# Kernel tuning notes

Hardware: AMD Instinct MI355X
Metric: run time of the kernel (lower is better)

## Reference

```python
import jax, jax.numpy as jnp
import numpy as np

CODEBOOK_SIZE = 8192
TOKEN_SIZE = 256
COMMITMENT_COST = 0.25
B, C, H, W = 32, 256, 32, 32


def setup_inputs() -> dict:
    key = jax.random.key(0)
    k1, k2 = jax.random.split(key)
    z = jax.random.normal(k1, (B, C, H, W), dtype=jnp.float32)
    # torch init: uniform_(-1/codebook_size, 1/codebook_size)
    embedding = jax.random.uniform(
        k2, (CODEBOOK_SIZE, TOKEN_SIZE), dtype=jnp.float32,
        minval=-1.0 / CODEBOOK_SIZE, maxval=1.0 / CODEBOOK_SIZE)
    return {"z": z, "embedding": embedding}


def reference(z, embedding):
    # b c h w -> b h w c
    z = jnp.transpose(z.astype(jnp.float32), (0, 2, 3, 1))
    b, h, w, c = z.shape
    z_flat = z.reshape(-1, c)  # [N, c]

    # squared euclidean distances: ||z||^2 + ||e||^2 - 2 z e^T
    d = (jnp.sum(z_flat ** 2, axis=1, keepdims=True)
         + jnp.sum(embedding ** 2, axis=1)
         - 2.0 * jnp.einsum('nd,kd->nk', z_flat, embedding))  # [N, K]
    idx = jnp.argmin(d, axis=1)  # [N]

    z_q = embedding[idx].reshape(z.shape)  # [b,h,w,c]

    commitment_loss = COMMITMENT_COST * jnp.mean(
        (jax.lax.stop_gradient(z_q) - z) ** 2)
    codebook_loss = jnp.mean((z_q - jax.lax.stop_gradient(z)) ** 2)
    loss = commitment_loss + codebook_loss

    # straight-through estimator
    z_q_st = z + jax.lax.stop_gradient(z_q - z)
    z_q_out = jnp.transpose(z_q_st, (0, 3, 1, 2))  # b h w c -> b c h w

    min_encoding_indices = idx.reshape(b, h, w)
    return (z_q_out, loss, commitment_loss, codebook_loss,
            min_encoding_indices)
```

## Files before the change

### kernel.cpp

```cpp
#include <hip/hip_runtime.h>
#include <float.h>

#define NBATCH 32
#define NCHAN  256
#define NHW    1024
#define NTOK   32768
#define NK     8192
#define ND     256
#define ZELEMS 8388608
#define OUT_LOSS 8388608
#define OUT_IDX  8388611
#define MARGIN   1.2e-4f

typedef short bf16x8  __attribute__((ext_vector_type(8)));
typedef float f32x4   __attribute__((ext_vector_type(4)));
typedef float f32x16  __attribute__((ext_vector_type(16)));

__device__ __forceinline__ unsigned short f2bf(float f) {
    unsigned int u = __float_as_uint(f);
    u += 0x7FFFu + ((u >> 16) & 1u);
    return (unsigned short)(u >> 16);
}

__device__ __forceinline__ float embed8(float x, int code) {
    return __int_as_float((__float_as_int(x) & 0xFFFFFF00) | code);
}


__global__ __launch_bounds__(256) void k_cast(const float* __restrict__ zg,
                                              const float* __restrict__ E,
                                              unsigned short* __restrict__ Epre,
                                              unsigned short* __restrict__ Zpre,
                                              float* __restrict__ en,
                                              float* __restrict__ acc,
                                              int* __restrict__ counter) {
    __shared__ unsigned short buf[128][34];
    const int t = threadIdx.x;
    if (blockIdx.x < 1024) {
        int g = blockIdx.x * 256 + t;
        int code = g >> 5, c16 = g & 31;
        int kc = c16 >> 2, ks = (c16 >> 1) & 1, lhi = c16 & 1;
        const float4* E4 = (const float4*)(E + code * ND + c16 * 8);
        float4 a = E4[0], b = E4[1];
        float s = a.x*a.x + a.y*a.y + a.z*a.z + a.w*a.w
                + b.x*b.x + b.y*b.y + b.z*b.z + b.w*b.w;
        #pragma unroll
        for (int off = 1; off < 32; off <<= 1) s += __shfl_xor(s, off, 64);
        if ((t & 31) == 0) en[code] = s;
        unsigned int u[4];
        u[0] = (unsigned int)f2bf(a.x) | ((unsigned int)f2bf(a.y) << 16);
        u[1] = (unsigned int)f2bf(a.z) | ((unsigned int)f2bf(a.w) << 16);
        u[2] = (unsigned int)f2bf(b.x) | ((unsigned int)f2bf(b.y) << 16);
        u[3] = (unsigned int)f2bf(b.z) | ((unsigned int)f2bf(b.w) << 16);
        *(uint4*)((char*)Epre + (size_t)(code >> 7) * 65536 + kc * 8192
                  + (ks * 2 + lhi) * 2048 + (code & 127) * 16) =
            make_uint4(u[0], u[1], u[2], u[3]);
        if (blockIdx.x == 0 && t == 0) { acc[0] = 0.0f; counter[0] = 0; }
    } else {
        int bi = blockIdx.x - 1024;
        int b = bi >> 6, kc = (bi >> 3) & 7, hwt = bi & 7;
        int c0 = kc * 32, hw0 = hwt * 128;
        #pragma unroll
        for (int r = 0; r < 4; ++r) {
            int idx = r * 256 + t;
            int c = idx >> 5, q = idx & 31;
            float4 v = *(const float4*)&zg[(b * 256 + c0 + c) * 1024 + hw0 + q * 4];
            buf[q * 4 + 0][c] = f2bf(v.x);
            buf[q * 4 + 1][c] = f2bf(v.y);
            buf[q * 4 + 2][c] = f2bf(v.z);
            buf[q * 4 + 3][c] = f2bf(v.w);
        }
        __syncthreads();
        int tok = t >> 1, ks = t & 1;
        char* base = (char*)Zpre + (size_t)((b * 8 + hwt) * 8 + kc) * 8192;
        #pragma unroll
        for (int lhi = 0; lhi < 2; ++lhi) {
            unsigned int u[4];
            #pragma unroll
            for (int k = 0; k < 4; ++k) {
                int cc = ks * 16 + lhi * 8 + 2 * k;
                u[k] = (unsigned int)buf[tok][cc] | ((unsigned int)buf[tok][cc + 1] << 16);
            }
            *(uint4*)(base + (ks * 2 + lhi) * 2048 + tok * 16) =
                make_uint4(u[0], u[1], u[2], u[3]);
        }
    }
}

__global__ __launch_bounds__(256, 2) void k_dist(const unsigned short* __restrict__ Epre,
                                                 const unsigned short* __restrict__ Zpre,
                                                 const float* __restrict__ en,
                                                 float2* __restrict__ part2) {
    __shared__ __align__(16) char Elds[3][16384];
    __shared__ __align__(16) char Zlds[3][8192];
    __shared__ float2 red[2][128];
    __shared__ float en_s[256];

    const int t    = threadIdx.x;
    const int kbb2 = blockIdx.x;
    const int mb   = blockIdx.y;
    const int n0   = mb * 128;
    const int w    = t >> 6, lane = t & 63;
    const int l31  = lane & 31, lhi = lane >> 5;
    const int wm   = w >> 1, wn = w & 1;

    const char* Esrc = (const char*)Epre + (size_t)kbb2 * 131072;
    const char* Zsrc = (const char*)Zpre + (size_t)mb * 65536;

    float en_v = en[kbb2 * 256 + t];

    auto STAGE = [&](int bb, int kc) {
        #pragma unroll
        for (int s = 0; s < 2; ++s)
            #pragma unroll
            for (int h = 0; h < 2; ++h)
                __builtin_amdgcn_global_load_lds(
                    (const unsigned int*)(Esrc + (size_t)s * 65536 + kc * 8192 + h * 4096 + t * 16),
                    (unsigned int*)&Elds[bb][s * 8192 + h * 4096 + t * 16], 16, 0, 0);
        #pragma unroll
        for (int h = 0; h < 2; ++h)
            __builtin_amdgcn_global_load_lds(
                (const unsigned int*)(Zsrc + kc * 8192 + h * 4096 + t * 16),
                (unsigned int*)&Zlds[bb][h * 4096 + t * 16], 16, 0, 0);
    };

    f32x16 acc[4][2];
    #pragma unroll
    for (int i = 0; i < 4; ++i)
        #pragma unroll
        for (int j = 0; j < 2; ++j) acc[i][j] = (f32x16)0.0f;

    STAGE(0, 0);
    STAGE(1, 1);

    #pragma unroll
    for (int kc = 0; kc < 8; ++kc) {
        const int pp = kc % 3;
        if (kc < 7) { asm volatile("s_waitcnt vmcnt(6)" ::: "memory"); }
        else        { asm volatile("s_waitcnt vmcnt(0)" ::: "memory"); }
        asm volatile("s_barrier" ::: "memory");
        if (kc < 6) STAGE((kc + 2) % 3, kc + 2);

        const char* Eb = &Elds[pp][0] + wm * 8192 + lhi * 2048 + l31 * 16;
        const char* Zb = &Zlds[pp][0] + lhi * 2048 + (wn * 64 + l31) * 16;
        bf16x8 ea[4][2], zb[2][2];
        #pragma unroll
        for (int i = 0; i < 4; ++i)
            #pragma unroll
            for (int ks = 0; ks < 2; ++ks)
                ea[i][ks] = *(const bf16x8*)(Eb + ks * 4096 + i * 512);
        #pragma unroll
        for (int j = 0; j < 2; ++j)
            #pragma unroll
            for (int ks = 0; ks < 2; ++ks)
                zb[j][ks] = *(const bf16x8*)(Zb + ks * 4096 + j * 512);
        __builtin_amdgcn_s_setprio(1);
        #pragma unroll
        for (int ks = 0; ks < 2; ++ks)
            #pragma unroll
            for (int i = 0; i < 4; ++i)
                #pragma unroll
                for (int j = 0; j < 2; ++j)
                    acc[i][j] = __builtin_amdgcn_mfma_f32_32x32x16_bf16(
                        ea[i][ks], zb[j][ks], acc[i][j], 0, 0, 0);
        __builtin_amdgcn_s_setprio(0);
    }

    en_s[t] = en_v;
    __syncthreads();

    float v1[2] = { FLT_MAX, FLT_MAX }, v2[2] = { FLT_MAX, FLT_MAX };
    #pragma unroll
    for (int i = 0; i < 4; ++i) {
        const int cb = wm * 128 + i * 32 + lhi * 4;
        #pragma unroll
        for (int rq = 0; rq < 4; ++rq) {
            f32x4 ev = *(const f32x4*)&en_s[cb + 8 * rq];
            #pragma unroll
            for (int rr = 0; rr < 4; ++rr) {
                const int r = rq * 4 + rr;
                const int code = cb + 8 * rq + rr;
                #pragma unroll
                for (int j = 0; j < 2; ++j) {
                    float s  = fmaf(-2.0f, acc[i][j][r], ev[rr]);
                    float se = embed8(s, code);
                    v2[j] = __builtin_amdgcn_fmed3f(se, v1[j], v2[j]);
                    v1[j] = fminf(v1[j], se);
                }
            }
        }
    }
    #pragma unroll
    for (int j = 0; j < 2; ++j) {
        float b1 = __shfl_xor(v1[j], 32, 64);
        float b2 = __shfl_xor(v2[j], 32, 64);
        float hi = fmaxf(v1[j], b1);
        v1[j] = fminf(v1[j], b1);
        v2[j] = fminf(fminf(hi, v2[j]), b2);
    }
    if (lane < 32) {
        #pragma unroll
        for (int j = 0; j < 2; ++j)
            red[wm][wn * 64 + j * 32 + l31] = make_float2(v1[j], v2[j]);
    }
    __syncthreads();
    if (t < 128) {
        float2 A = red[0][t], B = red[1][t];
        float g1 = fminf(A.x, B.x);
        float g2 = fminf(fminf(fmaxf(A.x, B.x), A.y), B.y);
        part2[(size_t)kbb2 * NTOK + n0 + t] = make_float2(g1, g2);
    }
}

__global__ __launch_bounds__(256) void k_refine(const float* __restrict__ zg,
                                                const float* __restrict__ E,
                                                const float2* __restrict__ part2,
                                                int* __restrict__ idxw,
                                                float* __restrict__ outF) {
    __shared__ float Zs[256 * 65];
    const int t = threadIdx.x;
    const int n0 = blockIdx.x * 64;
    const int b = n0 >> 10, hw0 = n0 & 1023;

    #pragma unroll
    for (int r = 0; r < 16; ++r) {
        int li = r * 256 + t;
        int c = li >> 4, q = li & 15;
        float4 v = *(const float4*)&zg[(b * 256 + c) * 1024 + hw0 + q * 4];
        Zs[c * 65 + q * 4 + 0] = v.x;
        Zs[c * 65 + q * 4 + 1] = v.y;
        Zs[c * 65 + q * 4 + 2] = v.z;
        Zs[c * 65 + q * 4 + 3] = v.w;
    }
    __syncthreads();

    const int w = t >> 6, l = t & 63;
    for (int it = 0; it < 16; ++it) {
        const int tokl = w * 16 + it;
        const int n = n0 + tokl;

        float zreg[4];
        #pragma unroll
        for (int j = 0; j < 4; ++j) zreg[j] = Zs[(64 * j + l) * 65 + tokl];

        double z2 = 0.0;
        #pragma unroll
        for (int j = 0; j < 4; ++j) z2 += (double)zreg[j] * (double)zreg[j];
        #pragma unroll
        for (int m = 1; m < 64; m <<= 1) z2 += __shfl_xor(z2, m, 64);
        const float z2f = (float)z2;

        float2 p = make_float2(FLT_MAX, FLT_MAX);
        if (l < 32) p = part2[(size_t)l * NTOK + n];
        int code1 = (l << 8) | (__float_as_int(p.x) & 0xFF);
        int code2 = (l << 8) | (__float_as_int(p.y) & 0xFF);

        float vmin = p.x;
        #pragma unroll
        for (int m = 1; m < 64; m <<= 1) vmin = fminf(vmin, __shfl_xor(vmin, m, 64));
        const float thr = vmin + MARGIN;

        unsigned long long m1 = __ballot(p.x <= thr);
        unsigned long long m2 = __ballot(p.y <= thr);

        float bdq = FLT_MAX; int bidx = 0x7fffffff;
        #pragma unroll
        for (int pass = 0; pass < 2; ++pass) {
            unsigned long long mm = pass ? m2 : m1;
            int ibits = pass ? code2 : code1;
            while (mm) {
                int src = __ffsll(mm) - 1; mm &= mm - 1;
                int cidx = __shfl(ibits, src, 64);
                const float* erow = E + cidx * ND;
                double g = (double)zreg[0] * (double)erow[l]
                         + (double)zreg[1] * (double)erow[64 + l]
                         + (double)zreg[2] * (double)erow[128 + l]
                         + (double)zreg[3] * (double)erow[192 + l];
                #pragma unroll
                for (int mk = 1; mk < 64; mk <<= 1) g += __shfl_xor(g, mk, 64);
                float c  = (float)(2.0 * g);
                float dq = z2f - c;
                if (dq < bdq || (dq == bdq && cidx < bidx)) { bdq = dq; bidx = cidx; }
            }
        }
        if (l == 0) { idxw[n] = bidx; outF[OUT_IDX + n] = (float)bidx; }
    }
}

__global__ __launch_bounds__(256) void k_gather(const float* __restrict__ E,
                                                const float* __restrict__ zg,
                                                const int* __restrict__ idxw,
                                                float* __restrict__ out,
                                                float* __restrict__ acc,
                                                int* __restrict__ counter) {
    __shared__ __align__(16) float Es[64 * 256];
    __shared__ int sidx[64];
    __shared__ float wred[4];
    const int t = threadIdx.x;
    const int b = blockIdx.x >> 4, ht = blockIdx.x & 15;

    if (t < 64) sidx[t] = idxw[b * 1024 + ht * 64 + t];
    __syncthreads();
    const float4* E4 = (const float4*)E;
    #pragma unroll
    for (int r = 0; r < 16; ++r) {
        int li = r * 256 + t;
        int row = li >> 6, slot = li & 63;
        float4 v = E4[(size_t)sidx[row] * 64 + slot];
        *(float4*)&Es[row * 256 + ((slot ^ (row & 15)) * 4)] = v;
    }
    __syncthreads();

    const int hw = t & 63, wv = t >> 6;
    float s = 0.0f;
    #pragma unroll 8
    for (int cc = 0; cc < 64; ++cc) {
        int c = wv * 64 + cc;
        float e = Es[hw * 256 + (((c >> 2) ^ (hw & 15)) * 4) + (c & 3)];
        size_t gi = (size_t)(b * 256 + c) * 1024 + ht * 64 + hw;
        float zv = zg[gi];
        out[gi] = e;
        float d = e - zv;
        s = fmaf(d, d, s);
    }
    #pragma unroll
    for (int off = 32; off > 0; off >>= 1) s += __shfl_down(s, off, 64);
    if ((t & 63) == 0) wred[wv] = s;
    __syncthreads();
    if (t == 0) {
        atomicAdd(acc, wred[0] + wred[1] + wred[2] + wred[3]);
        __threadfence();
        int old = atomicAdd(counter, 1);
        if (old == 511) {
            float total = atomicAdd(acc, 0.0f);
            float mse = total / 8388608.0f;
            out[OUT_LOSS + 0] = 1.25f * mse;
            out[OUT_LOSS + 1] = 0.25f * mse;
            out[OUT_LOSS + 2] = mse;
        }
    }
}

extern "C" void kernel_launch(void* const* d_in, const int* in_sizes, int n_in,
                              void* d_out, int out_size, void* d_ws, size_t ws_size,
                              hipStream_t stream) {
    const float* zg = (const float*)d_in[0];
    const float* E  = (const float*)d_in[1];
    float* out = (float*)d_out;
    float* wsf = (float*)d_ws;
    float*  acc     = wsf;
    int*    counter = (int*)(wsf + 1);
    float*  en      = wsf + 64;
    int*    idxw    = (int*)(wsf + 64 + NK);
    float2* part2   = (float2*)(wsf + 64 + NK + NTOK);
    unsigned short* Epre = (unsigned short*)(wsf + 64 + NK + NTOK + 4194304);
    unsigned short* Zpre = (unsigned short*)d_out;

    k_cast  <<<3072, 256, 0, stream>>>(zg, E, Epre, Zpre, en, acc, counter);
    k_dist  <<<dim3(32, 256), 256, 0, stream>>>(Epre, Zpre, en, part2);
    k_refine<<<NTOK / 64, 256, 0, stream>>>(zg, E, part2, idxw, out);
    k_gather<<<512, 256, 0, stream>>>(E, zg, idxw, out, acc, counter);
}
```

Measured before the change: 294.3 us.

## Double-buffer LDS fragment loads across k-slices and split min-reduction chains

Restructures the GEMM main loop into 16 half-chunk steps. The LDS fragment reads for the next k-slice are issued into a second register set while the current slice's MFMAs run. The codebook-norm vector is now loaded straight into LDS with an async global_load_lds at the start. The top-2 min tracking is split into four independent chains per column and merged afterwards, which shortens the serial dependency chain. The trade-off is higher register pressure from the doubled fragment registers and more complex waitcnt and barrier placement, which could cut occupancy or add stalls.

```diff
diff --git a/kernel.cpp b/kernel.cpp
--- a/kernel.cpp
+++ b/kernel.cpp
@@ -107,8 +107,6 @@
     const char* Esrc = (const char*)Epre + (size_t)kbb2 * 131072;
     const char* Zsrc = (const char*)Zpre + (size_t)mb * 65536;
 
-    float en_v = en[kbb2 * 256 + t];
-
     auto STAGE = [&](int bb, int kc) {
         #pragma unroll
         for (int s = 0; s < 2; ++s)
@@ -124,52 +122,61 @@
                 (unsigned int*)&Zlds[bb][h * 4096 + t * 16], 16, 0, 0);
     };
 
+    bf16x8 eaR[2][4], zbR[2][2];
+    const int ebase = wm * 8192 + lhi * 2048 + l31 * 16;
+    const int zbase = lhi * 2048 + (wn * 64 + l31) * 16;
+    auto LOADSLICE = [&](int set, int bb, int ks) {
+        const char* Eb = &Elds[bb][0] + ebase + ks * 4096;
+        const char* Zb = &Zlds[bb][0] + zbase + ks * 4096;
+        #pragma unroll
+        for (int i = 0; i < 4; ++i) eaR[set][i] = *(const bf16x8*)(Eb + i * 512);
+        #pragma unroll
+        for (int j = 0; j < 2; ++j) zbR[set][j] = *(const bf16x8*)(Zb + j * 512);
+    };
+
     f32x16 acc[4][2];
     #pragma unroll
     for (int i = 0; i < 4; ++i)
         #pragma unroll
         for (int j = 0; j < 2; ++j) acc[i][j] = (f32x16)0.0f;
 
+    __builtin_amdgcn_global_load_lds((const unsigned int*)(en + kbb2 * 256 + t),
+                                     (unsigned int*)&en_s[t], 4, 0, 0);
     STAGE(0, 0);
     STAGE(1, 1);
-
-    #pragma unroll
-    for (int kc = 0; kc < 8; ++kc) {
-        const int pp = kc % 3;
-        if (kc < 7) { asm volatile("s_waitcnt vmcnt(6)" ::: "memory"); }
-        else        { asm volatile("s_waitcnt vmcnt(0)" ::: "memory"); }
-        asm volatile("s_barrier" ::: "memory");
-        if (kc < 6) STAGE((kc + 2) % 3, kc + 2);
-
-        const char* Eb = &Elds[pp][0] + wm * 8192 + lhi * 2048 + l31 * 16;
-        const char* Zb = &Zlds[pp][0] + lhi * 2048 + (wn * 64 + l31) * 16;
-        bf16x8 ea[4][2], zb[2][2];
+    asm volatile("s_waitcnt vmcnt(6)" ::: "memory");
+    __builtin_amdgcn_s_barrier();
+    LOADSLICE(0, 0, 0);
+
+    #pragma unroll
+    for (int s = 0; s < 16; ++s) {
+        const int kc = s >> 1;
+        const int cs = s & 1, ns = cs ^ 1;
+        if ((s & 1) && kc < 6) STAGE((kc + 2) % 3, kc + 2);
+        if ((s & 1) && s < 15) {
+            if (s <= 11) { asm volatile("s_waitcnt vmcnt(6)" ::: "memory"); }
+            else         { asm volatile("s_waitcnt vmcnt(0)" ::: "memory"); }
+            asm volatile("s_waitcnt lgkmcnt(0)" ::: "memory");
+            __builtin_amdgcn_s_barrier();
+        }
+        if (s < 15) LOADSLICE(ns, ((s + 1) >> 1) % 3, (s + 1) & 1);
+        __builtin_amdgcn_s_setprio(1);
         #pragma unroll
         for (int i = 0; i < 4; ++i)
             #pragma unroll
-            for (int ks = 0; ks < 2; ++ks)
-                ea[i][ks] = *(const bf16x8*)(Eb + ks * 4096 + i * 512);
-        #pragma unroll
-        for (int j = 0; j < 2; ++j)
-            #pragma unroll
-            for (int ks = 0; ks < 2; ++ks)
-                zb[j][ks] = *(const bf16x8*)(Zb + ks * 4096 + j * 512);
-        __builtin_amdgcn_s_setprio(1);
-        #pragma unroll
-        for (int ks = 0; ks < 2; ++ks)
-            #pragma unroll
-            for (int i = 0; i < 4; ++i)
-                #pragma unroll
-                for (int j = 0; j < 2; ++j)
-                    acc[i][j] = __builtin_amdgcn_mfma_f32_32x32x16_bf16(
-                        ea[i][ks], zb[j][ks], acc[i][j], 0, 0, 0);
+            for (int j = 0; j < 2; ++j)
+                acc[i][j] = __builtin_amdgcn_mfma_f32_32x32x16_bf16(
+                    eaR[cs][i], zbR[cs][j], acc[i][j], 0, 0, 0);
         __builtin_amdgcn_s_setprio(0);
     }
 
-    en_s[t] = en_v;
-    __syncthreads();
-
-    float v1[2] = { FLT_MAX, FLT_MAX }, v2[2] = { FLT_MAX, FLT_MAX };
+    __syncthreads();
+
+    float v1[2][4], v2[2][4];
+    #pragma unroll
+    for (int j = 0; j < 2; ++j)
+        #pragma unroll
+        for (int i = 0; i < 4; ++i) { v1[j][i] = FLT_MAX; v2[j][i] = FLT_MAX; }
     #pragma unroll
     for (int i = 0; i < 4; ++i) {
         const int cb = wm * 128 + i * 32 + lhi * 4;
@@ -184,24 +191,36 @@
                 for (int j = 0; j < 2; ++j) {
                     float s  = fmaf(-2.0f, acc[i][j][r], ev[rr]);
                     float se = embed8(s, code);
-                    v2[j] = __builtin_amdgcn_fmed3f(se, v1[j], v2[j]);
-                    v1[j] = fminf(v1[j], se);
+                    v2[j][i] = __builtin_amdgcn_fmed3f(se, v1[j][i], v2[j][i]);
+                    v1[j][i] = fminf(v1[j][i], se);
                 }
             }
         }
     }
+    float m1[2], m2[2];
     #pragma unroll
     for (int j = 0; j < 2; ++j) {
-        float b1 = __shfl_xor(v1[j], 32, 64);
-        float b2 = __shfl_xor(v2[j], 32, 64);
-        float hi = fmaxf(v1[j], b1);
-        v1[j] = fminf(v1[j], b1);
-        v2[j] = fminf(fminf(hi, v2[j]), b2);
+        float a1 = fminf(v1[j][0], v1[j][1]);
+        float ah = fmaxf(v1[j][0], v1[j][1]);
+        float a2 = fminf(ah, fminf(v2[j][0], v2[j][1]));
+        float b1 = fminf(v1[j][2], v1[j][3]);
+        float bh = fmaxf(v1[j][2], v1[j][3]);
+        float b2 = fminf(bh, fminf(v2[j][2], v2[j][3]));
+        m1[j] = fminf(a1, b1);
+        m2[j] = fminf(fmaxf(a1, b1), fminf(a2, b2));
+    }
+    #pragma unroll
+    for (int j = 0; j < 2; ++j) {
+        float b1 = __shfl_xor(m1[j], 32, 64);
+        float b2 = __shfl_xor(m2[j], 32, 64);
+        float hi = fmaxf(m1[j], b1);
+        m1[j] = fminf(m1[j], b1);
+        m2[j] = fminf(fminf(hi, m2[j]), b2);
     }
     if (lane < 32) {
         #pragma unroll
         for (int j = 0; j < 2; ++j)
-            red[wm][wn * 64 + j * 32 + l31] = make_float2(v1[j], v2[j]);
+            red[wm][wn * 64 + j * 32 + l31] = make_float2(m1[j], m2[j]);
     }
     __syncthreads();
     if (t < 128) {
```

After: 295.9 us. About the same (+0.5%).

## Split k_dist tile across 8 waves with 512 threads per block

Applied to the files above, without the earlier changes.

Raises the distance-kernel block from 4 to 8 waves. Each wave now computes a 64x64 slice instead of 128x64, which halves its accumulator registers and allows four blocks per CU instead of two. The staging loads are spread across the extra threads, the codebook norms are loaded into LDS before the main loop, and the final min-reduction now combines four wave rows. The aim is more latency hiding through higher occupancy. The cost is more barrier participants per block and less operand reuse per wave.

```diff
diff --git a/kernel.cpp b/kernel.cpp
--- a/kernel.cpp
+++ b/kernel.cpp
@@ -87,13 +87,13 @@
     }
 }
 
-__global__ __launch_bounds__(256, 2) void k_dist(const unsigned short* __restrict__ Epre,
+__global__ __launch_bounds__(512, 4) void k_dist(const unsigned short* __restrict__ Epre,
                                                  const unsigned short* __restrict__ Zpre,
                                                  const float* __restrict__ en,
                                                  float2* __restrict__ part2) {
     __shared__ __align__(16) char Elds[3][16384];
     __shared__ __align__(16) char Zlds[3][8192];
-    __shared__ float2 red[2][128];
+    __shared__ float2 red[4][128];
     __shared__ float en_s[256];
 
     const int t    = threadIdx.x;
@@ -107,45 +107,46 @@
     const char* Esrc = (const char*)Epre + (size_t)kbb2 * 131072;
     const char* Zsrc = (const char*)Zpre + (size_t)mb * 65536;
 
-    float en_v = en[kbb2 * 256 + t];
-
     auto STAGE = [&](int bb, int kc) {
         #pragma unroll
-        for (int s = 0; s < 2; ++s)
-            #pragma unroll
-            for (int h = 0; h < 2; ++h)
-                __builtin_amdgcn_global_load_lds(
-                    (const unsigned int*)(Esrc + (size_t)s * 65536 + kc * 8192 + h * 4096 + t * 16),
-                    (unsigned int*)&Elds[bb][s * 8192 + h * 4096 + t * 16], 16, 0, 0);
-        #pragma unroll
-        for (int h = 0; h < 2; ++h)
+        for (int s2 = 0; s2 < 2; ++s2)
             __builtin_amdgcn_global_load_lds(
-                (const unsigned int*)(Zsrc + kc * 8192 + h * 4096 + t * 16),
-                (unsigned int*)&Zlds[bb][h * 4096 + t * 16], 16, 0, 0);
+                (const unsigned int*)(Esrc + (size_t)s2 * 65536 + kc * 8192 + t * 16),
+                (unsigned int*)&Elds[bb][s2 * 8192 + t * 16], 16, 0, 0);
+        __builtin_amdgcn_global_load_lds(
+            (const unsigned int*)(Zsrc + kc * 8192 + t * 16),
+            (unsigned int*)&Zlds[bb][t * 16], 16, 0, 0);
     };
 
-    f32x16 acc[4][2];
-    #pragma unroll
-    for (int i = 0; i < 4; ++i)
+    f32x16 acc[2][2];
+    #pragma unroll
+    for (int i = 0; i < 2; ++i)
         #pragma unroll
         for (int j = 0; j < 2; ++j) acc[i][j] = (f32x16)0.0f;
 
     STAGE(0, 0);
     STAGE(1, 1);
+    if (t < 256) en_s[t] = en[kbb2 * 256 + t];
+    __syncthreads();
+
+    const int eoff = (wm >> 1) * 8192 + (wm & 1) * 1024 + lhi * 2048 + l31 * 16;
+    const int zoff = lhi * 2048 + (wn * 64 + l31) * 16;
 
     #pragma unroll
     for (int kc = 0; kc < 8; ++kc) {
         const int pp = kc % 3;
-        if (kc < 7) { asm volatile("s_waitcnt vmcnt(6)" ::: "memory"); }
-        else        { asm volatile("s_waitcnt vmcnt(0)" ::: "memory"); }
-        asm volatile("s_barrier" ::: "memory");
+        if (kc >= 1) {
+            if (kc < 7) { asm volatile("s_waitcnt vmcnt(3)" ::: "memory"); }
+            else        { asm volatile("s_waitcnt vmcnt(0)" ::: "memory"); }
+            __builtin_amdgcn_s_barrier();
+        }
         if (kc < 6) STAGE((kc + 2) % 3, kc + 2);
 
-        const char* Eb = &Elds[pp][0] + wm * 8192 + lhi * 2048 + l31 * 16;
-        const char* Zb = &Zlds[pp][0] + lhi * 2048 + (wn * 64 + l31) * 16;
-        bf16x8 ea[4][2], zb[2][2];
-        #pragma unroll
-        for (int i = 0; i < 4; ++i)
+        const char* Eb = &Elds[pp][0] + eoff;
+        const char* Zb = &Zlds[pp][0] + zoff;
+        bf16x8 ea[2][2], zb[2][2];
+        #pragma unroll
+        for (int i = 0; i < 2; ++i)
             #pragma unroll
             for (int ks = 0; ks < 2; ++ks)
                 ea[i][ks] = *(const bf16x8*)(Eb + ks * 4096 + i * 512);
@@ -154,11 +155,12 @@
             #pragma unroll
             for (int ks = 0; ks < 2; ++ks)
                 zb[j][ks] = *(const bf16x8*)(Zb + ks * 4096 + j * 512);
+
         __builtin_amdgcn_s_setprio(1);
         #pragma unroll
         for (int ks = 0; ks < 2; ++ks)
             #pragma unroll
-            for (int i = 0; i < 4; ++i)
+            for (int i = 0; i < 2; ++i)
                 #pragma unroll
                 for (int j = 0; j < 2; ++j)
                     acc[i][j] = __builtin_amdgcn_mfma_f32_32x32x16_bf16(
@@ -166,13 +168,16 @@
         __builtin_amdgcn_s_setprio(0);
     }
 
-    en_s[t] = en_v;
-    __syncthreads();
-
-    float v1[2] = { FLT_MAX, FLT_MAX }, v2[2] = { FLT_MAX, FLT_MAX };
-    #pragma unroll
-    for (int i = 0; i < 4; ++i) {
-        const int cb = wm * 128 + i * 32 + lhi * 4;
+    __syncthreads();
+
+    float v1[2][2], v2[2][2];
+    #pragma unroll
+    for (int j = 0; j < 2; ++j)
+        #pragma unroll
+        for (int i = 0; i < 2; ++i) { v1[j][i] = FLT_MAX; v2[j][i] = FLT_MAX; }
+    #pragma unroll
+    for (int i = 0; i < 2; ++i) {
+        const int cb = wm * 64 + i * 32 + lhi * 4;
         #pragma unroll
         for (int rq = 0; rq < 4; ++rq) {
             f32x4 ev = *(const f32x4*)&en_s[cb + 8 * rq];
@@ -184,30 +189,42 @@
                 for (int j = 0; j < 2; ++j) {
                     float s  = fmaf(-2.0f, acc[i][j][r], ev[rr]);
                     float se = embed8(s, code);
-                    v2[j] = __builtin_amdgcn_fmed3f(se, v1[j], v2[j]);
-                    v1[j] = fminf(v1[j], se);
+                    v2[j][i] = __builtin_amdgcn_fmed3f(se, v1[j][i], v2[j][i]);
+                    v1[j][i] = fminf(v1[j][i], se);
                 }
             }
         }
     }
+    float m1[2], m2[2];
     #pragma unroll
     for (int j = 0; j < 2; ++j) {
-        float b1 = __shfl_xor(v1[j], 32, 64);
-        float b2 = __shfl_xor(v2[j], 32, 64);
-        float hi = fmaxf(v1[j], b1);
-        v1[j] = fminf(v1[j], b1);
-        v2[j] = fminf(fminf(hi, v2[j]), b2);
+        float a1 = fminf(v1[j][0], v1[j][1]);
+        float ah = fmaxf(v1[j][0], v1[j][1]);
+        m1[j] = a1;
+        m2[j] = fminf(ah, fminf(v2[j][0], v2[j][1]));
+    }
+    #pragma unroll
+    for (int j = 0; j < 2; ++j) {
+        float b1 = __shfl_xor(m1[j], 32, 64);
+        float b2 = __shfl_xor(m2[j], 32, 64);
+        float hi = fmaxf(m1[j], b1);
+        m1[j] = fminf(m1[j], b1);
+        m2[j] = fminf(fminf(hi, m2[j]), b2);
     }
     if (lane < 32) {
         #pragma unroll
         for (int j = 0; j < 2; ++j)
-            red[wm][wn * 64 + j * 32 + l31] = make_float2(v1[j], v2[j]);
+            red[wm][wn * 64 + j * 32 + l31] = make_float2(m1[j], m2[j]);
     }
     __syncthreads();
     if (t < 128) {
-        float2 A = red[0][t], B = red[1][t];
-        float g1 = fminf(A.x, B.x);
-        float g2 = fminf(fminf(fmaxf(A.x, B.x), A.y), B.y);
+        float2 A = red[0][t], B = red[1][t], C = red[2][t], D = red[3][t];
+        float ab1 = fminf(A.x, B.x);
+        float ab2 = fminf(fmaxf(A.x, B.x), fminf(A.y, B.y));
+        float cd1 = fminf(C.x, D.x);
+        float cd2 = fminf(fmaxf(C.x, D.x), fminf(C.y, D.y));
+        float g1 = fminf(ab1, cd1);
+        float g2 = fminf(fmaxf(ab1, cd1), fminf(ab2, cd2));
         part2[(size_t)kbb2 * NTOK + n0 + t] = make_float2(g1, g2);
     }
 }
@@ -357,7 +374,7 @@
     unsigned short* Zpre = (unsigned short*)d_out;
 
     k_cast  <<<3072, 256, 0, stream>>>(zg, E, Epre, Zpre, en, acc, counter);
-    k_dist  <<<dim3(32, 256), 256, 0, stream>>>(Epre, Zpre, en, part2);
+    k_dist  <<<dim3(32, 256), 512, 0, stream>>>(Epre, Zpre, en, part2);
     k_refine<<<NTOK / 64, 256, 0, stream>>>(zg, E, part2, idxw, out);
     k_gather<<<512, 256, 0, stream>>>(E, zg, idxw, out, acc, counter);
 }
```

Measured after the change: 299.5 us. No clear change (+1.8%).
